# Kernel optimization log

Measured on AMD Instinct MI355X. Metric: run time of the kernel, lower is better.

Reference implementation:

```python
import jax, jax.numpy as jnp
import numpy as np

B, H, W, C = 8, 32, 32, 512
NUM_HEADS = 8
NUM_GROUPS = 32
EPS = 1e-5
SKIP_SCALE = 1.0
HEAD_DIM = C // NUM_HEADS


def setup_inputs() -> dict:
    key = jax.random.key(0)
    ks = jax.random.split(key, 7)
    fan_in, fan_out = C, 3 * C
    lim_qkv = np.sqrt(6.0 / (fan_in + fan_out))
    lim_out = 1e-5 * np.sqrt(6.0 / (C + C))
    return {
        "x": jax.random.normal(ks[0], (B, H, W, C), jnp.float32),
        "norm_scale": jnp.ones((C,), jnp.float32),
        "norm_bias": jnp.zeros((C,), jnp.float32),
        "qkv_kernel": jax.random.uniform(ks[1], (C, NUM_HEADS, 3 * HEAD_DIM), jnp.float32, -lim_qkv, lim_qkv),
        "qkv_bias": jnp.zeros((NUM_HEADS, 3 * HEAD_DIM), jnp.float32),
        "out_kernel": jax.random.uniform(ks[2], (NUM_HEADS, HEAD_DIM, C), jnp.float32, -lim_out, lim_out),
        "out_bias": jnp.zeros((C,), jnp.float32),
    }


def group_norm(x, scale, bias):
    # x: (B, S, C); normalize per-group over (S, C//G), flax GroupNorm semantics
    b, s, c = x.shape
    g = NUM_GROUPS
    xg = x.reshape(b, s, g, c // g)
    mean = jnp.mean(xg, axis=(1, 3), keepdims=True)
    var = jnp.var(xg, axis=(1, 3), keepdims=True)
    xg = (xg - mean) * jax.lax.rsqrt(var + EPS)
    return xg.reshape(b, s, c) * scale + bias


def reference(x, norm_scale, norm_bias, qkv_kernel, qkv_bias, out_kernel, out_bias):
    batch_dims = x.shape[:-3]
    h, w, c = x.shape[-3:]
    xi = x.reshape(-1, h * w, c)  # (B, S, C)
    out = group_norm(xi, norm_scale, norm_bias)
    # QKV projection: (B,S,C) x (C, NH, 3*HD) -> (B,S,NH,3*HD)
    qkv = jnp.einsum('bsc,chd->bshd', out, qkv_kernel) + qkv_bias
    q, k, v = jnp.split(qkv, 3, axis=-1)  # each (B,S,NH,HD)
    scale = 1.0 / jnp.sqrt(jnp.sqrt(jnp.asarray(HEAD_DIM, jnp.float32)))
    q = q * scale
    k = k * scale
    attn = jnp.einsum('bqhd,bkhd->bhqk', q, k)
    attn = jax.nn.softmax(attn, axis=-1)
    o = jnp.einsum('bhqk,bkhd->bqhd', attn, v)
    o = jnp.einsum('bqhd,hdc->bqc', o, out_kernel) + out_bias
    o = (o + xi) * SKIP_SCALE
    return o.reshape((*batch_dims, h, w, c))
```

## Files before the change

### kernel.cpp

```cpp
#include <hip/hip_runtime.h>
#include <stdint.h>

typedef __attribute__((ext_vector_type(8))) short short8;
typedef __attribute__((ext_vector_type(4))) float f32x4;
typedef __attribute__((ext_vector_type(16))) float f32x16;
typedef __attribute__((ext_vector_type(4))) unsigned int u32x4;
typedef unsigned short u16;
typedef unsigned int u32;

#define NBATCH 8
#define SLEN 1024
#define CDIM 512
#define NHEADS 8
#define HDIM 64
#define MROWS (NBATCH*SLEN)
#define NQKV (NHEADS*3*HDIM)
#define QK_SCALE 0.35355339059327373f

__device__ inline u16 f2bf(float f){
  union{float f; uint32_t i;} v; v.f=f;
  uint32_t r = v.i + 0x7fffu + ((v.i>>16)&1u);
  return (u16)(r>>16);
}

__device__ inline u32 pk2(float a, float b){
  u32 r;
  asm("v_cvt_pk_bf16_f32 %0, %1, %2" : "=v"(r) : "v"(a), "v"(b));
  return r;
}

__device__ __forceinline__ void gld16(const u16* g, u16* l){
  __builtin_amdgcn_global_load_lds(
    (const __attribute__((address_space(1))) void*)g,
    (__attribute__((address_space(3))) void*)l, 16, 0, 0);
}

template<int N>
__global__ __launch_bounds__(256) void prep_w(const float* __restrict__ w, u16* __restrict__ wt){
  int tk = blockIdx.x / (N/64), tn = blockIdx.x % (N/64);
  int k0 = tk*64, n0 = tn*64;
  int t = threadIdx.x;
  __shared__ u16 lt[64][72];
  int row = t >> 2, slot = t & 3;
  const float* src = w + (size_t)(k0+row)*N + n0 + slot*16;
  #pragma unroll
  for (int j=0;j<16;++j)
    lt[row][slot*16+j] = f2bf(src[j]);
  __syncthreads();
  u16 tmp[16];
  #pragma unroll
  for (int j=0;j<16;++j) tmp[j] = lt[slot*16+j][row];
  *(u32x4*)(wt + (size_t)(n0+row)*512 + k0 + slot*16)     = *(u32x4*)tmp;
  *(u32x4*)(wt + (size_t)(n0+row)*512 + k0 + slot*16 + 8) = *(u32x4*)(tmp+8);
}

__global__ __launch_bounds__(256) void gn_stats(const float* __restrict__ x, float* __restrict__ stats){
  int bid = blockIdx.x;
  int b = bid >> 5, g = bid & 31;
  int t = threadIdx.x;
  const float* base = x + (size_t)b*SLEN*CDIM + g*16;
  float s1=0.f, s2=0.f;
  for (int s = t; s < SLEN; s += 256){
    const float4* p = (const float4*)(base + (size_t)s*CDIM);
    #pragma unroll
    for (int j=0;j<4;++j){
      float4 v = p[j];
      s1 += v.x+v.y+v.z+v.w;
      s2 += v.x*v.x + v.y*v.y + v.z*v.z + v.w*v.w;
    }
  }
  #pragma unroll
  for (int m=1;m<64;m<<=1){ s1 += __shfl_xor(s1,m); s2 += __shfl_xor(s2,m); }
  __shared__ float red[8];
  int wid = t>>6;
  if ((t&63)==0){ red[wid*2]=s1; red[wid*2+1]=s2; }
  __syncthreads();
  if (t==0){
    float a=0,c=0;
    #pragma unroll
    for (int w2=0;w2<4;++w2){ a+=red[w2*2]; c+=red[w2*2+1]; }
    float mean = a*(1.f/16384.f);
    float var  = c*(1.f/16384.f) - mean*mean;
    stats[bid*2]   = mean;
    stats[bid*2+1] = rsqrtf(var + 1e-5f);
  }
}

__global__ __launch_bounds__(256) void norm_cast(const float* __restrict__ x, const float* __restrict__ stats,
                        const float* __restrict__ scale, const float* __restrict__ bias,
                        u16* __restrict__ xn){
  int idx = blockIdx.x*256 + threadIdx.x;
  int m = idx >> 5, g = idx & 31;
  int b = m >> 10;
  float mean = stats[(b*32+g)*2];
  float rstd = stats[(b*32+g)*2+1];
  const float* xp = x + (size_t)m*CDIM + g*16;
  const float* sp = scale + g*16;
  const float* bp = bias + g*16;
  short8 o0, o1;
  #pragma unroll
  for (int j=0;j<16;++j){
    float v = (xp[j]-mean)*rstd*sp[j] + bp[j];
    if (j<8) o0[j] = (short)f2bf(v); else o1[j-8] = (short)f2bf(v);
  }
  short8* dst = (short8*)(xn + (size_t)m*CDIM + g*16);
  dst[0]=o0; dst[1]=o1;
}

#define BM 128
#define BN 128
#define BK 64

template<int EPI, int NT>
__global__ __launch_bounds__(256, 3) void gemm_bf16(
    const u16* __restrict__ A, const u16* __restrict__ Bt,
    const float* __restrict__ bias, const float* __restrict__ resid,
    float* __restrict__ outF,
    u16* __restrict__ qb, u16* __restrict__ kb, u16* __restrict__ vtb)
{
  const int K = CDIM;
  int t = threadIdx.x;
  int l = t & 63, wid = t >> 6;
  int g = l >> 4, c = l & 15;
  int wr = wid >> 1, wc = wid & 1;
  int nwg = gridDim.x;
  int cpx = nwg >> 3;
  int orig = blockIdx.x;
  int swz = (orig & 7)*cpx + (orig >> 3);
  int m0 = (swz / NT) * BM, n0 = (swz % NT) * BN;

  __shared__ __attribute__((aligned(16))) u16 ls[16384];
  char* lsAc = (char*)ls; char* lsBc = (char*)(ls + 8192);

  f32x4 acc[4][4];
  #pragma unroll
  for (int i=0;i<4;++i)
    #pragma unroll
    for(int j=0;j<4;++j) acc[i][j] = (f32x4)0.f;

  int lrow = l >> 3, slot = l & 7;
  int scol = ((slot ^ lrow) << 3);
  const int KT = K / BK;
  for (int kt=0; kt<KT; ++kt){
    __syncthreads();
    int kbo = kt*BK;
    #pragma unroll
    for (int q2=0; q2<4; ++q2){
      int row = wid*32 + q2*8 + lrow;
      gld16(A  + (size_t)(m0+row)*K + kbo + scol, ls        + (wid*4+q2)*512);
      gld16(Bt + (size_t)(n0+row)*K + kbo + scol, ls + 8192 + (wid*4+q2)*512);
    }
    asm volatile("s_waitcnt vmcnt(0)" ::: "memory");
    __syncthreads();
    #pragma unroll
    for (int kk=0; kk<2; ++kk){
      short8 af[4], bfr[4];
      #pragma unroll
      for (int i=0;i<4;++i){
        int rowA = wr*64 + i*16 + c;
        af[i]  = *(const short8*)(lsAc + rowA*128 + ((kk*4+g) ^ (rowA&7))*16);
        int rowB = wc*64 + i*16 + c;
        bfr[i] = *(const short8*)(lsBc + rowB*128 + ((kk*4+g) ^ (rowB&7))*16);
      }
      #pragma unroll
      for (int i=0;i<4;++i)
        #pragma unroll
        for (int j=0;j<4;++j)
          acc[i][j] = __builtin_amdgcn_mfma_f32_16x16x32_bf16(af[i], bfr[j], acc[i][j], 0,0,0);
    }
  }

  if (EPI == 0){
    int b = m0 >> 10, s0 = m0 & (SLEN-1);
    __syncthreads();
    u16* lsC = ls;
    #pragma unroll
    for (int i=0;i<4;++i){
      int rl0 = wr*64 + i*16 + g*4;
      #pragma unroll
      for (int j=0;j<4;++j){
        int cl = wc*64 + j*16 + c;
        int gcol = n0 + cl;
        int jj = gcol % 192;
        float sc_ = (jj < 128) ? QK_SCALE : 1.0f;
        float bv = bias[gcol];
        #pragma unroll
        for (int r=0;r<4;++r)
          lsC[(rl0+r)*128 + cl] = f2bf((acc[i][j][r] + bv)*sc_);
      }
    }
    __syncthreads();
    #pragma unroll
    for (int cc=0; cc<8; ++cc){
      int ch = cc*256 + t;
      int rl = ch >> 4, slot2 = ch & 15;
      int cl = slot2*8;
      int gcol = n0 + cl;
      int h = gcol / 192, jj = gcol % 192;
      int s = s0 + rl;
      u32x4 vv = *(const u32x4*)(lsC + rl*128 + cl);
      size_t rowb = ((size_t)(b*NHEADS+h))*SLEN + s;
      if (jj < 64)       __builtin_nontemporal_store(vv, (u32x4*)(qb + rowb*HDIM + jj));
      else if (jj < 128) __builtin_nontemporal_store(vv, (u32x4*)(kb + rowb*HDIM + (jj-64)));
    }
    int blk3 = (n0 >> 7) % 3;
    if (blk3 != 0){
      __syncthreads();
      u16* lsV = ls;
      #pragma unroll
      for (int i=0;i<4;++i){
        int rl0 = wr*64 + i*16 + g*4;
        #pragma unroll
        for (int j=0;j<4;++j){
          int cl = wc*64 + j*16 + c;
          int jj = (n0 + cl) % 192;
          if (jj >= 128){
            #pragma unroll
            for (int r=0;r<4;++r)
              lsV[(jj-128)*136 + rl0 + r] = f2bf(acc[i][j][r] + bias[n0+cl]);
          }
        }
      }
      __syncthreads();
      int hv = (n0 + ((blk3==1)?0:64)) / 192;
      size_t vbase = ((size_t)(b*NHEADS+hv))*HDIM*SLEN;
      #pragma unroll
      for (int cc=0; cc<4; ++cc){
        int chunk = cc*256 + t;
        int d = chunk >> 4, so = (chunk & 15)*8;
        u32x4 vv = *(const u32x4*)(lsV + d*136 + so);
        __builtin_nontemporal_store(vv, (u32x4*)(vtb + vbase + (size_t)d*SLEN + s0 + so));
      }
    }
  } else {
    #pragma unroll
    for (int i=0;i<4;++i){
      int grow = m0 + wr*64 + i*16 + g*4;
      #pragma unroll
      for (int j=0;j<4;++j){
        int gcol = n0 + wc*64 + j*16 + c;
        float bv = bias[gcol];
        #pragma unroll
        for (int r=0;r<4;++r){
          size_t off = (size_t)(grow+r)*CDIM + gcol;
          float rv = __builtin_nontemporal_load(&resid[off]);
          __builtin_nontemporal_store(acc[i][j][r] + bv + rv, &outF[off]);
        }
      }
    }
  }
}

#define PV_KS(PT, QOFF, V0, V1, KS) { \
    u32 A0 = pk2(PT[QOFF+0], PT[QOFF+1]); \
    u32 A1 = pk2(PT[QOFF+2], PT[QOFF+3]); \
    u32 B0 = pk2(PT[QOFF+4], PT[QOFF+5]); \
    u32 B1 = pk2(PT[QOFF+6], PT[QOFF+7]); \
    auto r0_ = __builtin_amdgcn_permlane32_swap((int)A0, (int)B0, false, false); \
    auto r1_ = __builtin_amdgcn_permlane32_swap((int)A1, (int)B1, false, false); \
    uint4 w; \
    w.x = (u32)r0_[0]; w.y = (u32)r1_[0]; w.z = (u32)r0_[1]; w.w = (u32)r1_[1]; \
    short8 fP; __builtin_memcpy(&fP, &w, 16); \
    o0 = __builtin_amdgcn_mfma_f32_32x32x16_bf16(V0[KS], fP, o0, 0,0,0); \
    o1 = __builtin_amdgcn_mfma_f32_32x32x16_bf16(V1[KS], fP, o1, 0,0,0); }

__global__ __launch_bounds__(256, 2) void attn_fused(const u16* __restrict__ qg,
  const u16* __restrict__ kg, const u16* __restrict__ vtg, u16* __restrict__ og)
{
  int bid = blockIdx.x;
  int nid = (bid & 7)*64 + (bid >> 3);
  int bh = nid >> 3, qi = nid & 7;
  int t = threadIdx.x, l = t & 63, wid = t >> 6;
  int q = l & 31, hi = l >> 5;
  int q0 = qi*128 + wid*32;

  __shared__ __attribute__((aligned(16))) u16 kl[4][4096];
  __shared__ __attribute__((aligned(16))) u16 vl[4][4096];

  const u16* qrow = qg + ((size_t)bh*SLEN + q0 + q)*HDIM + hi*8;
  short8 fQ[4];
  #pragma unroll
  for (int ds=0; ds<4; ++ds) fQ[ds] = *(const short8*)(qrow + ds*16);

  f32x16 o0, o1;
  #pragma unroll
  for (int r=0;r<16;++r){ o0[r]=0.f; o1[r]=0.f; }
  float mr = -1e30f, lsum = 0.f;

  const u16* kt_base = kg  + (size_t)bh*SLEN*HDIM;
  const u16* vt_base = vtg + (size_t)bh*HDIM*SLEN;
  int srow = l >> 3, sslot = l & 7;
  int scol8 = ((sslot ^ srow) << 3);

#define STAGE(BUF, KV) { \
    _Pragma("unroll") \
    for (int j=0;j<2;++j){ \
      int row = wid*16 + j*8 + srow; \
      int chunk = wid*2 + j; \
      gld16(kt_base + (size_t)((KV)*64 + row)*HDIM + scol8, &kl[BUF][chunk*512]); \
      gld16(vt_base + (size_t)row*SLEN + (KV)*64 + scol8,   &vl[BUF][chunk*512]); \
    } }

  STAGE(0, 0)
  STAGE(1, 1)
  STAGE(2, 2)
  STAGE(3, 3)

  int sl_q = q & 7;
  for (int p=0; p<8; ++p){
    if (p < 7) asm volatile("s_waitcnt vmcnt(8)" ::: "memory");
    else       asm volatile("s_waitcnt vmcnt(0)" ::: "memory");
    __syncthreads();
    int tA = 2*p, tB = 2*p+1;
    const u16* kA = &kl[tA&3][0]; const u16* kB = &kl[tB&3][0];
    const u16* vA = &vl[tA&3][0]; const u16* vB = &vl[tB&3][0];
    short8 fKA0[4], fKA1[4], fKB0[4], fKB1[4];
    #pragma unroll
    for (int ds=0; ds<4; ++ds){
      int sl = ((ds*2+hi) ^ sl_q) << 3;
      fKA0[ds] = *(const short8*)(kA + q*64 + sl);
      fKA1[ds] = *(const short8*)(kA + (q+32)*64 + sl);
      fKB0[ds] = *(const short8*)(kB + q*64 + sl);
      fKB1[ds] = *(const short8*)(kB + (q+32)*64 + sl);
    }
    f32x16 pA0, pA1, pB0, pB1;
    #pragma unroll
    for (int r=0;r<16;++r){ pA0[r]=0.f; pA1[r]=0.f; pB0[r]=0.f; pB1[r]=0.f; }
    __builtin_amdgcn_s_setprio(1);
    #pragma unroll
    for (int ds=0; ds<4; ++ds){
      pA0 = __builtin_amdgcn_mfma_f32_32x32x16_bf16(fKA0[ds], fQ[ds], pA0, 0,0,0);
      pB0 = __builtin_amdgcn_mfma_f32_32x32x16_bf16(fKB0[ds], fQ[ds], pB0, 0,0,0);
      pA1 = __builtin_amdgcn_mfma_f32_32x32x16_bf16(fKA1[ds], fQ[ds], pA1, 0,0,0);
      pB1 = __builtin_amdgcn_mfma_f32_32x32x16_bf16(fKB1[ds], fQ[ds], pB1, 0,0,0);
    }
    __builtin_amdgcn_s_setprio(0);
    short8 fVA0[4], fVA1[4], fVB0[4], fVB1[4];
    #pragma unroll
    for (int ks=0; ks<4; ++ks){
      int sl = ((ks*2+hi) ^ sl_q) << 3;
      fVA0[ks] = *(const short8*)(vA + q*64 + sl);
      fVA1[ks] = *(const short8*)(vA + (q+32)*64 + sl);
      fVB0[ks] = *(const short8*)(vB + q*64 + sl);
      fVB1[ks] = *(const short8*)(vB + (q+32)*64 + sl);
    }
    float a8[8];
    #pragma unroll
    for (int r=0;r<8;++r){
      float ma = fmaxf(fmaxf(pA0[r],pA0[r+8]), fmaxf(pA1[r],pA1[r+8]));
      float mb = fmaxf(fmaxf(pB0[r],pB0[r+8]), fmaxf(pB1[r],pB1[r+8]));
      a8[r] = fmaxf(ma, mb);
    }
    #pragma unroll
    for (int s=4;s>0;s>>=1)
      #pragma unroll
      for (int r=0;r<4;++r) if (r<s) a8[r] = fmaxf(a8[r], a8[r+s]);
    auto rm_ = __builtin_amdgcn_permlane32_swap(
        __builtin_bit_cast(int, a8[0]), __builtin_bit_cast(int, a8[0]), false, false);
    float tmax = fmaxf(a8[0], fmaxf(__builtin_bit_cast(float, rm_[0]),
                                    __builtin_bit_cast(float, rm_[1])));
    if (!__all(tmax <= mr + 8.0f)){
      float mn = fmaxf(mr, tmax);
      float alpha = __expf(mr - mn);
      mr = mn;
      lsum *= alpha;
      #pragma unroll
      for (int r=0;r<16;++r){ o0[r]*=alpha; o1[r]*=alpha; }
    }
    #pragma unroll
    for (int r=0;r<16;++r){
      pA0[r] = __expf(pA0[r]-mr); pA1[r] = __expf(pA1[r]-mr);
      pB0[r] = __expf(pB0[r]-mr); pB1[r] = __expf(pB1[r]-mr);
    }
    float s8[8];
    #pragma unroll
    for (int r=0;r<8;++r)
      s8[r] = ((pA0[r]+pA0[r+8]) + (pA1[r]+pA1[r+8]))
            + ((pB0[r]+pB0[r+8]) + (pB1[r]+pB1[r+8]));
    #pragma unroll
    for (int s=4;s>0;s>>=1)
      #pragma unroll
      for (int r=0;r<4;++r) if (r<s) s8[r] += s8[r+s];
    auto rs_ = __builtin_amdgcn_permlane32_swap(
        __builtin_bit_cast(int, s8[0]), __builtin_bit_cast(int, s8[0]), false, false);
    lsum += __builtin_bit_cast(float, rs_[0]) + __builtin_bit_cast(float, rs_[1]);
    __builtin_amdgcn_s_setprio(1);
    PV_KS(pA0, 0, fVA0, fVA1, 0)
    PV_KS(pA0, 8, fVA0, fVA1, 1)
    PV_KS(pA1, 0, fVA0, fVA1, 2)
    PV_KS(pA1, 8, fVA0, fVA1, 3)
    PV_KS(pB0, 0, fVB0, fVB1, 0)
    PV_KS(pB0, 8, fVB0, fVB1, 1)
    PV_KS(pB1, 0, fVB0, fVB1, 2)
    PV_KS(pB1, 8, fVB0, fVB1, 3)
    __builtin_amdgcn_s_setprio(0);
    __syncthreads();
    if (p < 6){
      STAGE((2*p+4)&3, 2*p+4)
      STAGE((2*p+5)&3, 2*p+5)
    }
  }

  float inv = 1.f / lsum;
  int b = bh >> 3, h = bh & 7;
  u16* obase = og + ((size_t)b*SLEN + q0 + q)*CDIM + h*HDIM;
  #pragma unroll
  for (int pr=0; pr<8; ++pr){
    int d = ((2*pr)&3) + 8*(pr>>1) + 4*hi;
    *(u32*)(obase + d)      = pk2(o0[2*pr]*inv, o0[2*pr+1]*inv);
    *(u32*)(obase + 32 + d) = pk2(o1[2*pr]*inv, o1[2*pr+1]*inv);
  }
}

extern "C" void kernel_launch(void* const* d_in, const int* in_sizes, int n_in,
                              void* d_out, int out_size, void* d_ws, size_t ws_size,
                              hipStream_t stream){
  const float* x      = (const float*)d_in[0];
  const float* nscale = (const float*)d_in[1];
  const float* nbias  = (const float*)d_in[2];
  const float* wqkv   = (const float*)d_in[3];
  const float* bqkv   = (const float*)d_in[4];
  const float* wout   = (const float*)d_in[5];
  const float* bout   = (const float*)d_in[6];
  float* out = (float*)d_out;

  char* ws = (char*)d_ws;
  size_t off = 0;
  auto alloc = [&](size_t bytes){ void* p = ws + off; off += (bytes + 255) & ~255ull; return p; };
  float* stats  = (float*)alloc(256*2*sizeof(float));
  u16* wqkv_t = (u16*)alloc((size_t)NQKV*CDIM*2);
  u16* wout_t = (u16*)alloc((size_t)CDIM*CDIM*2);
  u16* xn     = (u16*)alloc((size_t)MROWS*CDIM*2);
  u16* qb     = (u16*)alloc((size_t)MROWS*CDIM*2);
  u16* kb     = (u16*)alloc((size_t)MROWS*CDIM*2);
  u16* vtb    = (u16*)alloc((size_t)MROWS*CDIM*2);
  u16* ob     = (u16*)alloc((size_t)MROWS*CDIM*2);

  prep_w<NQKV><<<dim3(8*(NQKV/64)), dim3(256), 0, stream>>>(wqkv, wqkv_t);
  prep_w<CDIM><<<dim3(8*(CDIM/64)), dim3(256), 0, stream>>>(wout, wout_t);
  gn_stats <<<dim3(256), dim3(256), 0, stream>>>(x, stats);
  norm_cast<<<dim3((MROWS*32)/256), dim3(256), 0, stream>>>(x, stats, nscale, nbias, xn);
  gemm_bf16<0,12><<<dim3(768), dim3(256), 0, stream>>>(xn, wqkv_t, bqkv, nullptr, nullptr, qb, kb, vtb);
  attn_fused<<<dim3(512), dim3(256), 0, stream>>>(qb, kb, vtb, ob);
  gemm_bf16<1,4><<<dim3(256), dim3(256), 0, stream>>>(ob, wout_t, bout, x, out, nullptr, nullptr, nullptr);
}
```

Before: 95.19 us.

## Pipeline GEMM K-loop with triple-buffered LDS, fuse groupnorm and weight-prep launches

The bf16 GEMM now uses BK=32 with a three-stage LDS ring, prefetching the next K tile via global_load_lds before computing the current one, which overlaps loads with MFMA work. Its swizzle is adjusted to the 64-byte row pitch. The two weight-transpose kernels are merged into one launch, and groupnorm stats plus normalize/cast are fused into a single kernel that re-reads x. This cuts launches and the stats round trip, but the fused groupnorm runs only 256 blocks and the pipeline syncs once per shorter K step.

Result: slower. 118.3 us (+24.3%).

```diff
diff --git a/kernel.cpp b/kernel.cpp
--- a/kernel.cpp
+++ b/kernel.cpp
@@ -35,11 +35,10 @@
     (__attribute__((address_space(3))) void*)l, 16, 0, 0);
 }
 
-template<int N>
-__global__ __launch_bounds__(256) void prep_w(const float* __restrict__ w, u16* __restrict__ wt){
-  int tk = blockIdx.x / (N/64), tn = blockIdx.x % (N/64);
+__device__ __forceinline__ void prep_body(const float* __restrict__ w, u16* __restrict__ wt,
+                                          int N, int blk, int t){
+  int tk = blk / (N/64), tn = blk % (N/64);
   int k0 = tk*64, n0 = tn*64;
-  int t = threadIdx.x;
   __shared__ u16 lt[64][72];
   int row = t >> 2, slot = t & 3;
   const float* src = w + (size_t)(k0+row)*N + n0 + slot*16;
@@ -54,11 +53,21 @@
   *(u32x4*)(wt + (size_t)(n0+row)*512 + k0 + slot*16 + 8) = *(u32x4*)(tmp+8);
 }
 
-__global__ __launch_bounds__(256) void gn_stats(const float* __restrict__ x, float* __restrict__ stats){
+__global__ __launch_bounds__(256) void prep_all(const float* __restrict__ wqkv, const float* __restrict__ wout,
+                                                u16* __restrict__ wqkv_t, u16* __restrict__ wout_t){
+  int blk = blockIdx.x, t = threadIdx.x;
+  if (blk < 8*(NQKV/64)) prep_body(wqkv, wqkv_t, NQKV, blk, t);
+  else                   prep_body(wout, wout_t, CDIM, blk - 8*(NQKV/64), t);
+}
+
+__global__ __launch_bounds__(256) void gn_fused(const float* __restrict__ x,
+                        const float* __restrict__ scale, const float* __restrict__ bias,
+                        u16* __restrict__ xn){
   int bid = blockIdx.x;
   int b = bid >> 5, g = bid & 31;
   int t = threadIdx.x;
   const float* base = x + (size_t)b*SLEN*CDIM + g*16;
+  u16* obase = xn + (size_t)b*SLEN*CDIM + g*16;
   float s1=0.f, s2=0.f;
   for (int s = t; s < SLEN; s += 256){
     const float4* p = (const float4*)(base + (size_t)s*CDIM);
@@ -72,6 +81,7 @@
   #pragma unroll
   for (int m=1;m<64;m<<=1){ s1 += __shfl_xor(s1,m); s2 += __shfl_xor(s2,m); }
   __shared__ float red[8];
+  __shared__ float mv[2];
   int wid = t>>6;
   if ((t&63)==0){ red[wid*2]=s1; red[wid*2+1]=s2; }
   __syncthreads();
@@ -81,35 +91,29 @@
     for (int w2=0;w2<4;++w2){ a+=red[w2*2]; c+=red[w2*2+1]; }
     float mean = a*(1.f/16384.f);
     float var  = c*(1.f/16384.f) - mean*mean;
-    stats[bid*2]   = mean;
-    stats[bid*2+1] = rsqrtf(var + 1e-5f);
-  }
-}
-
-__global__ __launch_bounds__(256) void norm_cast(const float* __restrict__ x, const float* __restrict__ stats,
-                        const float* __restrict__ scale, const float* __restrict__ bias,
-                        u16* __restrict__ xn){
-  int idx = blockIdx.x*256 + threadIdx.x;
-  int m = idx >> 5, g = idx & 31;
-  int b = m >> 10;
-  float mean = stats[(b*32+g)*2];
-  float rstd = stats[(b*32+g)*2+1];
-  const float* xp = x + (size_t)m*CDIM + g*16;
-  const float* sp = scale + g*16;
-  const float* bp = bias + g*16;
-  short8 o0, o1;
-  #pragma unroll
-  for (int j=0;j<16;++j){
-    float v = (xp[j]-mean)*rstd*sp[j] + bp[j];
-    if (j<8) o0[j] = (short)f2bf(v); else o1[j-8] = (short)f2bf(v);
-  }
-  short8* dst = (short8*)(xn + (size_t)m*CDIM + g*16);
-  dst[0]=o0; dst[1]=o1;
+    mv[0] = mean; mv[1] = rsqrtf(var + 1e-5f);
+  }
+  __syncthreads();
+  float mean = mv[0], rstd = mv[1];
+  float sc[16], bi[16];
+  #pragma unroll
+  for (int j=0;j<16;++j){ sc[j] = scale[g*16+j]*rstd; bi[j] = bias[g*16+j] - mean*scale[g*16+j]*rstd; }
+  for (int s = t; s < SLEN; s += 256){
+    const float* xp = base + (size_t)s*CDIM;
+    short8 o0, o1;
+    #pragma unroll
+    for (int j=0;j<16;++j){
+      float v = xp[j]*sc[j] + bi[j];
+      if (j<8) o0[j] = (short)f2bf(v); else o1[j-8] = (short)f2bf(v);
+    }
+    short8* dst = (short8*)(obase + (size_t)s*CDIM);
+    dst[0]=o0; dst[1]=o1;
+  }
 }
 
 #define BM 128
 #define BN 128
-#define BK 64
+#define BK 32
 
 template<int EPI, int NT>
 __global__ __launch_bounds__(256, 3) void gemm_bf16(
@@ -129,8 +133,7 @@
   int swz = (orig & 7)*cpx + (orig >> 3);
   int m0 = (swz / NT) * BM, n0 = (swz % NT) * BN;
 
-  __shared__ __attribute__((aligned(16))) u16 ls[16384];
-  char* lsAc = (char*)ls; char* lsBc = (char*)(ls + 8192);
+  __shared__ __attribute__((aligned(16))) u16 ls[3][8192];
 
   f32x4 acc[4][4];
   #pragma unroll
@@ -138,42 +141,48 @@
     #pragma unroll
     for(int j=0;j<4;++j) acc[i][j] = (f32x4)0.f;
 
-  int lrow = l >> 3, slot = l & 7;
-  int scol = ((slot ^ lrow) << 3);
+  int lrow = l >> 2, lslot = l & 3;
+  int scol = ((lslot ^ (lrow & 3) ^ ((lrow >> 2) & 3)) << 3);
+
+#define STAGE_G(BUF, KT_) { \
+    _Pragma("unroll") \
+    for (int j=0;j<2;++j){ \
+      int ch = wid*2 + j; \
+      int row = ch*16 + lrow; \
+      gld16(A  + (size_t)(m0+row)*K + (KT_)*BK + scol, &ls[BUF][ch*512]); \
+      gld16(Bt + (size_t)(n0+row)*K + (KT_)*BK + scol, &ls[BUF][4096 + ch*512]); \
+    } }
+
   const int KT = K / BK;
+  STAGE_G(0, 0)
+  int slot_read = (g ^ (c & 3) ^ ((c >> 2) & 3));
   for (int kt=0; kt<KT; ++kt){
+    if (kt+1 < KT) STAGE_G((kt+1)%3, kt+1)
+    if (kt+1 < KT) asm volatile("s_waitcnt vmcnt(4)" ::: "memory");
+    else           asm volatile("s_waitcnt vmcnt(0)" ::: "memory");
     __syncthreads();
-    int kbo = kt*BK;
-    #pragma unroll
-    for (int q2=0; q2<4; ++q2){
-      int row = wid*32 + q2*8 + lrow;
-      gld16(A  + (size_t)(m0+row)*K + kbo + scol, ls        + (wid*4+q2)*512);
-      gld16(Bt + (size_t)(n0+row)*K + kbo + scol, ls + 8192 + (wid*4+q2)*512);
-    }
-    asm volatile("s_waitcnt vmcnt(0)" ::: "memory");
-    __syncthreads();
-    #pragma unroll
-    for (int kk=0; kk<2; ++kk){
-      short8 af[4], bfr[4];
-      #pragma unroll
-      for (int i=0;i<4;++i){
-        int rowA = wr*64 + i*16 + c;
-        af[i]  = *(const short8*)(lsAc + rowA*128 + ((kk*4+g) ^ (rowA&7))*16);
-        int rowB = wc*64 + i*16 + c;
-        bfr[i] = *(const short8*)(lsBc + rowB*128 + ((kk*4+g) ^ (rowB&7))*16);
-      }
-      #pragma unroll
-      for (int i=0;i<4;++i)
-        #pragma unroll
-        for (int j=0;j<4;++j)
-          acc[i][j] = __builtin_amdgcn_mfma_f32_16x16x32_bf16(af[i], bfr[j], acc[i][j], 0,0,0);
-    }
-  }
-
+    const char* Ab = (const char*)&ls[kt%3][0];
+    const char* Bb = (const char*)&ls[kt%3][4096];
+    short8 af[4], bfr[4];
+    #pragma unroll
+    for (int i=0;i<4;++i){
+      int rowA = wr*64 + i*16 + c;
+      af[i]  = *(const short8*)(Ab + rowA*64 + slot_read*16);
+      int rowB = wc*64 + i*16 + c;
+      bfr[i] = *(const short8*)(Bb + rowB*64 + slot_read*16);
+    }
+    #pragma unroll
+    for (int i=0;i<4;++i)
+      #pragma unroll
+      for (int j=0;j<4;++j)
+        acc[i][j] = __builtin_amdgcn_mfma_f32_16x16x32_bf16(af[i], bfr[j], acc[i][j], 0,0,0);
+  }
+
+  u16* lsf = &ls[0][0];
   if (EPI == 0){
     int b = m0 >> 10, s0 = m0 & (SLEN-1);
     __syncthreads();
-    u16* lsC = ls;
+    u16* lsC = lsf;
     #pragma unroll
     for (int i=0;i<4;++i){
       int rl0 = wr*64 + i*16 + g*4;
@@ -206,7 +215,7 @@
     int blk3 = (n0 >> 7) % 3;
     if (blk3 != 0){
       __syncthreads();
-      u16* lsV = ls;
+      u16* lsV = lsf;
       #pragma unroll
       for (int i=0;i<4;++i){
         int rl0 = wr*64 + i*16 + g*4;
@@ -427,7 +436,6 @@
   char* ws = (char*)d_ws;
   size_t off = 0;
   auto alloc = [&](size_t bytes){ void* p = ws + off; off += (bytes + 255) & ~255ull; return p; };
-  float* stats  = (float*)alloc(256*2*sizeof(float));
   u16* wqkv_t = (u16*)alloc((size_t)NQKV*CDIM*2);
   u16* wout_t = (u16*)alloc((size_t)CDIM*CDIM*2);
   u16* xn     = (u16*)alloc((size_t)MROWS*CDIM*2);
@@ -436,10 +444,8 @@
   u16* vtb    = (u16*)alloc((size_t)MROWS*CDIM*2);
   u16* ob     = (u16*)alloc((size_t)MROWS*CDIM*2);
 
-  prep_w<NQKV><<<dim3(8*(NQKV/64)), dim3(256), 0, stream>>>(wqkv, wqkv_t);
-  prep_w<CDIM><<<dim3(8*(CDIM/64)), dim3(256), 0, stream>>>(wout, wout_t);
-  gn_stats <<<dim3(256), dim3(256), 0, stream>>>(x, stats);
-  norm_cast<<<dim3((MROWS*32)/256), dim3(256), 0, stream>>>(x, stats, nscale, nbias, xn);
+  prep_all<<<dim3(8*(NQKV/64) + 8*(CDIM/64)), dim3(256), 0, stream>>>(wqkv, wout, wqkv_t, wout_t);
+  gn_fused<<<dim3(256), dim3(256), 0, stream>>>(x, nscale, nbias, xn);
   gemm_bf16<0,12><<<dim3(768), dim3(256), 0, stream>>>(xn, wqkv_t, bqkv, nullptr, nullptr, qb, kb, vtb);
   attn_fused<<<dim3(512), dim3(256), 0, stream>>>(qb, kb, vtb, ob);
   gemm_bf16<1,4><<<dim3(256), dim3(256), 0, stream>>>(ob, wout_t, bout, x, out, nullptr, nullptr, nullptr);
```
